# Optimization experiments

Hardware: AMD Instinct MI355X
Metric: run time of the kernel (lower is better)

## Reference

```python
import math
import jax, jax.numpy as jnp
import numpy as np

B, T = 2, 2048
D_MODEL, D_HEAD = 2048, 128
N_Q, N_KV = 16, 4
QPG = N_Q // N_KV  # queries per kv group
ROPE_BASE = 10000.0
YARN_SCALE = 4.0
ORIG_MAX_LEN = 4096
BETA_FAST, BETA_SLOW = 32.0, 1.0
RMS_EPS = 1.1920929e-07  # torch.finfo(float32).eps (nn.RMSNorm default)


def _yarn_inv_freq():
    inv = 1.0 / ROPE_BASE ** (np.arange(0, D_HEAD, 2, dtype=np.float32) / D_HEAD)
    wavelengths = 2.0 * math.pi / inv
    low_wavelen = ORIG_MAX_LEN / BETA_SLOW
    high_wavelen = ORIG_MAX_LEN / BETA_FAST
    gamma = np.clip((low_wavelen - wavelengths) / (low_wavelen - high_wavelen), 0.0, 1.0)
    return (gamma * inv + (1.0 - gamma) * inv / YARN_SCALE).astype(np.float32)

INV_FREQ = jnp.asarray(_yarn_inv_freq())  # (D_HEAD//2,) constant buffer
MSCALE = 0.1 * math.log(YARN_SCALE) + 1.0
ATTN_SCALE = 1.0 / (MSCALE * math.sqrt(D_HEAD))


def _rms_norm(x, w):
    # normalize over last dim (d_head), learnable per-dim weight
    return x * jax.lax.rsqrt(jnp.mean(x * x, axis=-1, keepdims=True) + RMS_EPS) * w


def _apply_rope(x):
    # x: (..., T, d_head)
    t = jnp.arange(x.shape[-2], dtype=jnp.float32)
    freqs = jnp.outer(t, INV_FREQ)                 # (T, d/2)
    emb = jnp.concatenate([freqs, freqs], axis=-1)  # (T, d)
    cos, sin = jnp.cos(emb), jnp.sin(emb)
    half = x.shape[-1] // 2
    x_rot = jnp.concatenate([-x[..., half:], x[..., :half]], axis=-1)
    return x * cos + x_rot * sin


def setup_inputs() -> dict:
    key = jax.random.key(0)
    ks = jax.random.split(key, 5)
    x = jax.random.normal(ks[0], (B, T, D_MODEL), dtype=jnp.float32)
    w_scale = 0.02
    Wq = jax.random.normal(ks[1], (D_MODEL, N_Q * D_HEAD), dtype=jnp.float32) * w_scale
    Wkv = jax.random.normal(ks[2], (D_MODEL, 2 * N_KV * D_HEAD), dtype=jnp.float32) * w_scale
    Wo = jax.random.normal(ks[3], (N_Q * D_HEAD, D_MODEL), dtype=jnp.float32) * w_scale
    q_norm_w = jnp.ones((D_HEAD,), dtype=jnp.float32)
    k_norm_w = jnp.ones((D_HEAD,), dtype=jnp.float32)
    return {"x": x, "Wq": Wq, "Wkv": Wkv, "Wo": Wo,
            "q_norm_w": q_norm_w, "k_norm_w": k_norm_w}


def reference(x, Wq, Wkv, Wo, q_norm_w, k_norm_w):
    b, t, _ = x.shape
    # projections
    q = (x @ Wq).reshape(b, t, QPG, N_KV, D_HEAD).transpose(0, 2, 3, 1, 4)  # (b,qpg,g,t,d)
    kv = x @ Wkv
    k, v = jnp.split(kv, 2, axis=-1)
    k = k.reshape(b, t, N_KV, D_HEAD).transpose(0, 2, 1, 3)  # (b,g,t,d)
    v = v.reshape(b, t, N_KV, D_HEAD).transpose(0, 2, 1, 3)  # (b,g,t,d)
    # RMSNorm + YaRN RoPE on q,k (math done in float32 as in source)
    q = _apply_rope(_rms_norm(q, q_norm_w))
    k = _apply_rope(_rms_norm(k, k_norm_w))
    # GQA replication: head index h = qpg*N_KV + g (matches source rearrange/reshape)
    q = q.reshape(b, N_Q, t, D_HEAD)
    k = jnp.broadcast_to(k[:, None], (b, QPG, N_KV, t, D_HEAD)).reshape(b, N_Q, t, D_HEAD)
    v = jnp.broadcast_to(v[:, None], (b, QPG, N_KV, t, D_HEAD)).reshape(b, N_Q, t, D_HEAD)
    # causal SDPA with custom scale
    scores = jnp.einsum('bhtd,bhsd->bhts', q, k) * ATTN_SCALE
    causal = jnp.tril(jnp.ones((t, t), dtype=bool))
    scores = jnp.where(causal, scores, jnp.finfo(scores.dtype).min)
    probs = jax.nn.softmax(scores, axis=-1)
    attn = jnp.einsum('bhts,bhsd->bhtd', probs, v)
    out = attn.transpose(0, 2, 1, 3).reshape(b, t, N_Q * D_HEAD)
    return out @ Wo
```

## Files before the change

### kernel.cpp

```cpp
#include <hip/hip_runtime.h>
#include <cmath>

typedef float f32x4 __attribute__((ext_vector_type(4)));
typedef float f32x16 __attribute__((ext_vector_type(16)));
typedef __bf16 bf16x8 __attribute__((ext_vector_type(8)));

#define DEV static __device__ __forceinline__

DEV unsigned short f2bf(float f) {
  unsigned int u = __builtin_bit_cast(unsigned int, f);
  u += 0x7FFFu + ((u >> 16) & 1u);
  return (unsigned short)(u >> 16);
}
DEV float bf2f(unsigned short h) {
  unsigned int u = ((unsigned int)h) << 16;
  return __builtin_bit_cast(float, u);
}
DEV unsigned int cvtpk(float lo, float hi) {
  unsigned int r;
  asm("v_cvt_pk_bf16_f32 %0, %1, %2" : "=v"(r) : "v"(lo), "v"(hi));
  return r;
}
DEV f32x4 mfma16(bf16x8 a, bf16x8 b, f32x4 c) {
  return __builtin_amdgcn_mfma_f32_16x16x32_bf16(a, b, c, 0, 0, 0);
}
DEV f32x16 mfma32(bf16x8 a, bf16x8 b, f32x16 c) {
  return __builtin_amdgcn_mfma_f32_32x32x16_bf16(a, b, c, 0, 0, 0);
}
DEV void dma16(const void* g, void* l) {
  __builtin_amdgcn_global_load_lds(
      (const __attribute__((address_space(1))) void*)(uintptr_t)g,
      (__attribute__((address_space(3))) void*)(unsigned int)(uintptr_t)l,
      16, 0, 0);
}

constexpr int T_SEQ = 2048;

__global__ __launch_bounds__(256) void build_rope(float2* __restrict__ rope) {
  int gid = blockIdx.x * 256 + threadIdx.x;
  if (gid >= T_SEQ * 64) return;
  int t = gid >> 6, i = gid & 63;
  double inv = pow(10000.0, -((double)(2 * i)) / 128.0);
  double wl = 6.283185307179586 / inv;
  double gm = (4096.0 - wl) / (4096.0 - 128.0);
  gm = gm < 0.0 ? 0.0 : (gm > 1.0 ? 1.0 : gm);
  float f = (float)(gm * inv + (1.0 - gm) * inv * 0.25);
  float th = (float)t * f;
  float s, c;
  sincosf(th, &s, &c);
  rope[gid] = make_float2(c, s);
}

__global__ __launch_bounds__(256) void cvt_f32_bf16(const float4* __restrict__ in,
                                                    ushort* __restrict__ out, int n4) {
  int i = blockIdx.x * 256 + threadIdx.x;
  if (i >= n4) return;
  float4 v = in[i];
  unsigned int lo = (unsigned int)f2bf(v.x) | ((unsigned int)f2bf(v.y) << 16);
  unsigned int hi = (unsigned int)f2bf(v.z) | ((unsigned int)f2bf(v.w) << 16);
  int row = i >> 9;
  int e = (i * 4) & 2047;
  size_t o = ((size_t)row << 11) + (size_t)(e ^ ((row & 7) << 3));
  *(uint2*)(out + o) = make_uint2(lo, hi);
}

__global__ __launch_bounds__(256) void tconv(const float* __restrict__ in,
                                             ushort* __restrict__ out, int R, int C) {
  __shared__ ushort tile[64][65];
  int c0 = blockIdx.x * 64, r0 = blockIdx.y * 64;
  int j = threadIdx.x & 63, i0 = threadIdx.x >> 6;
#pragma unroll
  for (int ii = 0; ii < 16; ++ii) {
    int i = i0 + ii * 4;
    tile[i][j] = f2bf(in[(size_t)(r0 + i) * C + c0 + j]);
  }
  __syncthreads();
#pragma unroll
  for (int ii = 0; ii < 16; ++ii) {
    int jr = i0 + ii * 4;
    out[(size_t)(c0 + jr) * R + ((r0 + j) ^ ((jr & 7) << 3))] = tile[j][jr];
  }
}

template <int OUT_BF16>
__global__ __launch_bounds__(256) void gemm_bt(const ushort* __restrict__ A,
                                               const ushort* __restrict__ Bt,
                                               void* __restrict__ Cv,
                                               int M, int N, int K) {
  __shared__ ushort lA[128 * 64];
  __shared__ ushort lB[128 * 64];
  const int tid = threadIdx.x;
  const int lane = tid & 63;
  const int w = tid >> 6;
  const int m0 = blockIdx.y * 128;
  const int n0 = blockIdx.x * 128;
  const int wm = (w >> 1) << 6;
  const int wn = (w & 1) << 6;

  f32x4 acc[4][4] = {};

  const size_t K2 = (size_t)K * 2;
  const char* Ab = (const char*)A + (size_t)m0 * K2;
  const char* Bb = (const char*)Bt + (size_t)n0 * K2;
  const int drow = w * 32 + (lane >> 3);
  const int dcb = (lane & 7) * 16;

  for (int k0 = 0; k0 < K; k0 += 64) {
#pragma unroll
    for (int ii = 0; ii < 4; ++ii) {
      const int off = w * 4096 + ii * 1024;
      const size_t gofs = (size_t)(drow + ii * 8) * K2 + (size_t)k0 * 2 + dcb;
      dma16(Ab + gofs, (char*)lA + off);
      dma16(Bb + gofs, (char*)lB + off);
    }
    __syncthreads();
#pragma unroll
    for (int kc = 0; kc < 2; ++kc) {
      bf16x8 a[4], bb[4];
#pragma unroll
      for (int mt = 0; mt < 4; ++mt) {
        int row = wm + mt * 16 + (lane & 15);
        int byo = kc * 64 + ((lane >> 4) << 4);
        a[mt] = *(const bf16x8*)((const char*)lA + row * 128 + (byo ^ ((row & 7) << 4)));
      }
#pragma unroll
      for (int nt = 0; nt < 4; ++nt) {
        int row = wn + nt * 16 + (lane & 15);
        int byo = kc * 64 + ((lane >> 4) << 4);
        bb[nt] = *(const bf16x8*)((const char*)lB + row * 128 + (byo ^ ((row & 7) << 4)));
      }
#pragma unroll
      for (int mt = 0; mt < 4; ++mt)
#pragma unroll
        for (int nt = 0; nt < 4; ++nt)
          acc[mt][nt] = mfma16(a[mt], bb[nt], acc[mt][nt]);
    }
    __syncthreads();
  }

  const int rr = (lane >> 4) << 2;
  const int cc = lane & 15;
  if (OUT_BF16) {
    ushort* C = (ushort*)Cv;
#pragma unroll
    for (int mt = 0; mt < 4; ++mt)
#pragma unroll
      for (int nt = 0; nt < 4; ++nt)
#pragma unroll
        for (int j = 0; j < 4; ++j) {
          int r = m0 + wm + mt * 16 + rr + j;
          int c = n0 + wn + nt * 16 + cc;
          C[(size_t)r * N + c] = f2bf(acc[mt][nt][j]);
        }
  } else {
    float* C = (float*)Cv;
#pragma unroll
    for (int mt = 0; mt < 4; ++mt)
#pragma unroll
      for (int nt = 0; nt < 4; ++nt)
#pragma unroll
        for (int j = 0; j < 4; ++j) {
          int r = m0 + wm + mt * 16 + rr + j;
          int c = n0 + wn + nt * 16 + cc;
          C[(size_t)r * N + c] = acc[mt][nt][j];
        }
  }
}

__global__ __launch_bounds__(256) void norm_rope(const ushort* __restrict__ qkv,
                                                 const float* __restrict__ qw,
                                                 const float* __restrict__ kw,
                                                 const float2* __restrict__ rope,
                                                 ushort* __restrict__ qout,
                                                 ushort* __restrict__ kout,
                                                 float q_scale) {
  const int w = threadIdx.x >> 6, lane = threadIdx.x & 63;
  const int vi = blockIdx.x * 4 + w;
  const ushort* src;
  const float* wt;
  ushort* dst;
  float extra;
  int t, bb;
  if (vi < 65536) {
    int row = vi >> 4, H = vi & 15;
    bb = row >> 11;
    t = row & 2047;
    src = qkv + (size_t)row * 3072 + H * 128 + lane * 2;
    wt = qw;
    extra = q_scale;
    dst = qout + ((size_t)(bb * 16 + H) * T_SEQ + t) * 128 + lane * 2;
  } else {
    int vi2 = vi - 65536;
    int row = vi2 >> 2, gg = vi2 & 3;
    bb = row >> 11;
    t = row & 2047;
    src = qkv + (size_t)row * 3072 + 2048 + gg * 128 + lane * 2;
    wt = kw;
    extra = 1.f;
    dst = kout + ((size_t)(bb * 4 + gg) * T_SEQ + t) * 128 +
          ((lane * 2) ^ ((t & 7) << 3));
  }
  float x0 = bf2f(src[0]), x1 = bf2f(src[1]);
  float ss = x0 * x0 + x1 * x1;
#pragma unroll
  for (int d = 1; d < 64; d <<= 1) ss += __shfl_xor(ss, d, 64);
  float sc = rsqrtf(ss * (1.f / 128.f) + 1.1920929e-7f);
  float w0 = wt[lane * 2], w1 = wt[lane * 2 + 1];
  float xn0 = x0 * sc * w0, xn1 = x1 * sc * w1;
  float p0 = __shfl_xor(xn0, 32, 64), p1 = __shfl_xor(xn1, 32, 64);
  float r0 = lane < 32 ? -p0 : p0;
  float r1 = lane < 32 ? -p1 : p1;
  int i0 = (lane * 2) & 63;
  float2 cs0 = rope[t * 64 + i0];
  float2 cs1 = rope[t * 64 + i0 + 1];
  float o0 = (xn0 * cs0.x + r0 * cs0.y) * extra;
  float o1 = (xn1 * cs1.x + r1 * cs1.y) * extra;
  unsigned int pk = (unsigned int)f2bf(o0) | ((unsigned int)f2bf(o1) << 16);
  *(unsigned int*)dst = pk;
}

__global__ __launch_bounds__(256) void tv_kernel(const ushort* __restrict__ qkv,
                                                 ushort* __restrict__ vt) {
  __shared__ ushort tile[64][65];
  int t0 = blockIdx.x * 64;
  int y = blockIdx.y;
  int dh = y & 1, bg = y >> 1;
  int bb = bg >> 2, g = bg & 3;
  int j = threadIdx.x & 63, i0 = threadIdx.x >> 6;
#pragma unroll
  for (int ii = 0; ii < 16; ++ii) {
    int i = i0 + ii * 4;
    tile[i][j] = qkv[(size_t)(bb * T_SEQ + t0 + i) * 3072 + 2560 + g * 128 + dh * 64 + j];
  }
  __syncthreads();
#pragma unroll
  for (int ii = 0; ii < 16; ++ii) {
    int jr = i0 + ii * 4;
    vt[((size_t)bg * 128 + dh * 64 + jr) * T_SEQ + ((t0 + j) ^ ((jr & 7) << 3))] = tile[j][jr];
  }
}

#define MKPA(P, B)                                                      \
  ({                                                                    \
    unsigned X1 = cvtpk(P[B + 0], P[B + 1]);                            \
    unsigned X2 = cvtpk(P[B + 2], P[B + 3]);                            \
    unsigned Y1 = cvtpk(P[B + 4], P[B + 5]);                            \
    unsigned Y2 = cvtpk(P[B + 6], P[B + 7]);                            \
    asm("v_permlane32_swap_b32 %0, %1" : "+v"(X1), "+v"(Y1));           \
    asm("v_permlane32_swap_b32 %0, %1" : "+v"(X2), "+v"(Y2));           \
    uint4 u4 = {X1, X2, Y1, Y2};                                        \
    __builtin_bit_cast(bf16x8, u4);                                     \
  })

__global__ __launch_bounds__(256, 2) void attn_fwd(const ushort* __restrict__ qh,
                                                   const ushort* __restrict__ kh,
                                                   const ushort* __restrict__ vt,
                                                   ushort* __restrict__ o) {
  const int f = blockIdx.x;
  const int half = f >> 8, c = f & 255;
  const int kk = c >> 5, bh = c & 31;
  const int qt = half ? kk : (15 - kk);
  const int b = bh >> 4, H = bh & 15;
  const int g = H & 3;
  const int tid = threadIdx.x, lane = tid & 63, w = tid >> 6;
  const int hi = lane >> 5;
  const int ql = lane & 31;
  const int wrow0 = qt * 128 + w * 32;

  __shared__ ushort lK[2][64 * 128];
  __shared__ ushort lV[2][128 * 64];

  bf16x8 qf[8];
  {
    const ushort* qb = qh + ((size_t)(b * 16 + H) * T_SEQ + wrow0 + ql) * 128 + 8 * hi;
#pragma unroll
    for (int cc = 0; cc < 8; ++cc) qf[cc] = *(const bf16x8*)(qb + 16 * cc);
  }

  f32x16 oacc[4] = {};
  float mrow = -INFINITY, lrow = 0.f;

  const char* kpl = (const char*)(kh + (size_t)(b * 4 + g) * T_SEQ * 128);
  const char* vpl = (const char*)(vt + (size_t)(b * 4 + g) * 128 * T_SEQ);

  auto stage = [&](int j, int bi) {
#pragma unroll
    for (int ii = 0; ii < 4; ++ii) {
      const int off = w * 4096 + ii * 1024;
      dma16(kpl + (size_t)j * 16384 + off + lane * 16, (char*)lK[bi] + off);
      const int vrow = w * 32 + ii * 8 + (lane >> 3);
      dma16(vpl + (size_t)vrow * (T_SEQ * 2) + j * 128 + (lane & 7) * 16,
            (char*)lV[bi] + off);
    }
  };

  stage(0, 0);

  const int swK = (ql & 7) << 4;
  const int jmax = 2 * qt + 1;

  for (int j = 0; j <= jmax; ++j) {
    const int cur = j & 1;
    if (j < jmax) {
      stage(j + 1, cur ^ 1);
      asm volatile("s_waitcnt vmcnt(8)" ::: "memory");
    } else {
      asm volatile("s_waitcnt vmcnt(0)" ::: "memory");
    }
    __builtin_amdgcn_s_barrier();
    __builtin_amdgcn_sched_barrier(0);

    const char* lKc = (const char*)lK[cur];
    const char* lVc = (const char*)lV[cur];

    f32x16 s0 = {}, s1 = {};
    __builtin_amdgcn_s_setprio(1);
#pragma unroll
    for (int cc = 0; cc < 8; ++cc) {
      bf16x8 kf = *(const bf16x8*)(lKc + ql * 256 + ((32 * cc + 16 * hi) ^ swK));
      s0 = mfma32(kf, qf[cc], s0);
    }
#pragma unroll
    for (int cc = 0; cc < 8; ++cc) {
      bf16x8 kf = *(const bf16x8*)(lKc + (32 + ql) * 256 + ((32 * cc + 16 * hi) ^ swK));
      s1 = mfma32(kf, qf[cc], s1);
    }
    __builtin_amdgcn_s_setprio(0);

    if (j * 64 + 63 > wrow0) {
      const int q = wrow0 + ql;
      const int kvb = j * 64 + 4 * hi;
#pragma unroll
      for (int r = 0; r < 16; ++r) {
        const int kv0 = kvb + (r & 3) + 8 * (r >> 2);
        if (kv0 > q) s0[r] = -3.0e38f;
        if (kv0 + 32 > q) s1[r] = -3.0e38f;
      }
    }

    float tm[8];
#pragma unroll
    for (int r = 0; r < 8; ++r)
      tm[r] = fmaxf(fmaxf(s0[r], s0[r + 8]), fmaxf(s1[r], s1[r + 8]));
    float pm = fmaxf(fmaxf(fmaxf(tm[0], tm[1]), fmaxf(tm[2], tm[3])),
                     fmaxf(fmaxf(tm[4], tm[5]), fmaxf(tm[6], tm[7])));
    pm = fmaxf(pm, __shfl_xor(pm, 32, 64));

    float mn = mrow;
    if (!__all(pm <= mrow + 11.5417f)) {
      mn = fmaxf(mrow, pm);
      float rsc = exp2f(mrow - mn);
      mrow = mn;
      lrow *= rsc;
#pragma unroll
      for (int r = 0; r < 16; ++r) {
        float rv = __shfl(rsc, (r & 3) + 8 * (r >> 2) + 4 * hi, 64);
#pragma unroll
        for (int n = 0; n < 4; ++n) oacc[n][r] *= rv;
      }
    }

    f32x16 p0, p1;
#pragma unroll
    for (int r = 0; r < 16; ++r) {
      p0[r] = exp2f(s0[r] - mn);
      p1[r] = exp2f(s1[r] - mn);
    }
    float ta[8];
#pragma unroll
    for (int r = 0; r < 8; ++r) ta[r] = (p0[r] + p0[r + 8]) + (p1[r] + p1[r + 8]);
    float ps = ((ta[0] + ta[1]) + (ta[2] + ta[3])) + ((ta[4] + ta[5]) + (ta[6] + ta[7]));
    ps += __shfl_xor(ps, 32, 64);
    lrow += ps;

    bf16x8 pa0 = MKPA(p0, 0), pa1 = MKPA(p0, 8);
    bf16x8 pa2 = MKPA(p1, 0), pa3 = MKPA(p1, 8);

    __builtin_amdgcn_s_setprio(1);
#pragma unroll
    for (int n = 0; n < 4; ++n) {
      const int row = 32 * n + ql;
      const int swV = (row & 7) << 4;
      const char* vb = lVc + row * 128;
      bf16x8 vf0 = *(const bf16x8*)(vb + ((16 * hi) ^ swV));
      bf16x8 vf1 = *(const bf16x8*)(vb + ((32 + 16 * hi) ^ swV));
      bf16x8 vf2 = *(const bf16x8*)(vb + ((64 + 16 * hi) ^ swV));
      bf16x8 vf3 = *(const bf16x8*)(vb + ((96 + 16 * hi) ^ swV));
      oacc[n] = mfma32(pa0, vf0, oacc[n]);
      oacc[n] = mfma32(pa1, vf1, oacc[n]);
      oacc[n] = mfma32(pa2, vf2, oacc[n]);
      oacc[n] = mfma32(pa3, vf3, oacc[n]);
    }
    __builtin_amdgcn_s_setprio(0);

    __builtin_amdgcn_sched_barrier(0);
    __builtin_amdgcn_s_barrier();
  }

  float linv = 1.f / lrow;
#pragma unroll
  for (int r = 0; r < 16; ++r) {
    const int qrr = (r & 3) + 8 * (r >> 2) + 4 * hi;
    float iv = __shfl(linv, qrr, 64);
    const int row = wrow0 + qrr;
    const size_t base = (size_t)(b * T_SEQ + row) * 2048;
    const int sw = (row & 7) << 3;
#pragma unroll
    for (int n = 0; n < 4; ++n) {
      int col = H * 128 + n * 32 + ql;
      o[base + (col ^ sw)] = f2bf(oacc[n][r] * iv);
    }
  }
}

extern "C" void kernel_launch(void* const* d_in, const int* in_sizes, int n_in,
                              void* d_out, int out_size, void* d_ws, size_t ws_size,
                              hipStream_t stream) {
  (void)in_sizes; (void)n_in; (void)out_size; (void)ws_size;
  const float* x = (const float*)d_in[0];
  const float* Wq = (const float*)d_in[1];
  const float* Wkv = (const float*)d_in[2];
  const float* Wo = (const float*)d_in[3];
  const float* qnw = (const float*)d_in[4];
  const float* knw = (const float*)d_in[5];
  float* out = (float*)d_out;
  char* ws = (char*)d_ws;

  ushort* xb = (ushort*)(ws);
  ushort* wqkv = (ushort*)(ws + 16777216);
  ushort* wot = (ushort*)(ws + 29360128);
  ushort* qkvraw = (ushort*)(ws + 37748736);
  ushort* kh = (ushort*)(ws + 62914560);
  ushort* vtp = (ushort*)(ws + 67108864);
  float2* rope = (float2*)(ws + 71303168);
  ushort* qh = xb;
  ushort* attnb = qkvraw;

  float attn_scale = 1.0f / ((0.1f * logf(4.0f) + 1.0f) * sqrtf(128.0f));
  float q_scale = attn_scale * 1.44269504f;

  build_rope<<<512, 256, 0, stream>>>(rope);
  cvt_f32_bf16<<<8192, 256, 0, stream>>>((const float4*)x, xb, 2097152);
  tconv<<<dim3(32, 32), 256, 0, stream>>>(Wq, wqkv, 2048, 2048);
  tconv<<<dim3(16, 32), 256, 0, stream>>>(Wkv, wqkv + (size_t)2048 * 2048, 2048, 1024);
  tconv<<<dim3(32, 32), 256, 0, stream>>>(Wo, wot, 2048, 2048);
  gemm_bt<1><<<dim3(24, 32), 256, 0, stream>>>(xb, wqkv, qkvraw, 4096, 3072, 2048);
  norm_rope<<<20480, 256, 0, stream>>>(qkvraw, qnw, knw, rope, qh, kh, q_scale);
  tv_kernel<<<dim3(32, 16), 256, 0, stream>>>(qkvraw, vtp);
  attn_fwd<<<512, 256, 0, stream>>>(qh, kh, vtp, attnb);
  gemm_bt<0><<<dim3(16, 32), 256, 0, stream>>>(attnb, wot, out, 4096, 2048, 2048);
}
```

Measured before the change: 228.6 us.

## Replace LDS-staged attention with single-wave blocks reading K/V from global

Attention is restructured from 256-thread blocks that double-buffer 64-key K/V tiles into shared memory via async DMA into 2048 single-wave blocks, each handling 32 query rows and reading 32-key K/V tiles straight from global memory. The shared-memory XOR swizzles on K and transposed V are removed from the producer kernels to match. This drops block barriers and LDS traffic and makes causal tiling finer, at the cost of no K/V reuse across the four waves of a block, more global/L2 traffic and exposed load latency without prefetch.

```diff
diff --git a/kernel.cpp b/kernel.cpp
--- a/kernel.cpp
+++ b/kernel.cpp
@@ -197,8 +197,7 @@
     src = qkv + (size_t)row * 3072 + 2048 + gg * 128 + lane * 2;
     wt = kw;
     extra = 1.f;
-    dst = kout + ((size_t)(bb * 4 + gg) * T_SEQ + t) * 128 +
-          ((lane * 2) ^ ((t & 7) << 3));
+    dst = kout + ((size_t)(bb * 4 + gg) * T_SEQ + t) * 128 + lane * 2;
   }
   float x0 = bf2f(src[0]), x1 = bf2f(src[1]);
   float ss = x0 * x0 + x1 * x1;
@@ -236,7 +235,7 @@
 #pragma unroll
   for (int ii = 0; ii < 16; ++ii) {
     int jr = i0 + ii * 4;
-    vt[((size_t)bg * 128 + dh * 64 + jr) * T_SEQ + ((t0 + j) ^ ((jr & 7) << 3))] = tile[j][jr];
+    vt[((size_t)bg * 128 + dh * 64 + jr) * T_SEQ + t0 + j] = tile[j][jr];
   }
 }
 
@@ -252,27 +251,23 @@
     __builtin_bit_cast(bf16x8, u4);                                     \
   })
 
-__global__ __launch_bounds__(256, 2) void attn_fwd(const ushort* __restrict__ qh,
-                                                   const ushort* __restrict__ kh,
-                                                   const ushort* __restrict__ vt,
-                                                   ushort* __restrict__ o) {
+__global__ __launch_bounds__(64) void attn_fwd(const ushort* __restrict__ qh,
+                                               const ushort* __restrict__ kh,
+                                               const ushort* __restrict__ vt,
+                                               ushort* __restrict__ o) {
   const int f = blockIdx.x;
-  const int half = f >> 8, c = f & 255;
-  const int kk = c >> 5, bh = c & 31;
-  const int qt = half ? kk : (15 - kk);
+  const int qs = 63 - (f >> 5);
+  const int bh = f & 31;
   const int b = bh >> 4, H = bh & 15;
   const int g = H & 3;
-  const int tid = threadIdx.x, lane = tid & 63, w = tid >> 6;
+  const int lane = threadIdx.x;
   const int hi = lane >> 5;
   const int ql = lane & 31;
-  const int wrow0 = qt * 128 + w * 32;
-
-  __shared__ ushort lK[2][64 * 128];
-  __shared__ ushort lV[2][128 * 64];
+  const int row0 = qs * 32;
 
   bf16x8 qf[8];
   {
-    const ushort* qb = qh + ((size_t)(b * 16 + H) * T_SEQ + wrow0 + ql) * 128 + 8 * hi;
+    const ushort* qb = qh + ((size_t)(b * 16 + H) * T_SEQ + row0 + ql) * 128 + 8 * hi;
 #pragma unroll
     for (int cc = 0; cc < 8; ++cc) qf[cc] = *(const bf16x8*)(qb + 16 * cc);
   }
@@ -280,68 +275,34 @@
   f32x16 oacc[4] = {};
   float mrow = -INFINITY, lrow = 0.f;
 
-  const char* kpl = (const char*)(kh + (size_t)(b * 4 + g) * T_SEQ * 128);
-  const char* vpl = (const char*)(vt + (size_t)(b * 4 + g) * 128 * T_SEQ);
-
-  auto stage = [&](int j, int bi) {
-#pragma unroll
-    for (int ii = 0; ii < 4; ++ii) {
-      const int off = w * 4096 + ii * 1024;
-      dma16(kpl + (size_t)j * 16384 + off + lane * 16, (char*)lK[bi] + off);
-      const int vrow = w * 32 + ii * 8 + (lane >> 3);
-      dma16(vpl + (size_t)vrow * (T_SEQ * 2) + j * 128 + (lane & 7) * 16,
-            (char*)lV[bi] + off);
-    }
-  };
-
-  stage(0, 0);
-
-  const int swK = (ql & 7) << 4;
-  const int jmax = 2 * qt + 1;
-
-  for (int j = 0; j <= jmax; ++j) {
-    const int cur = j & 1;
-    if (j < jmax) {
-      stage(j + 1, cur ^ 1);
-      asm volatile("s_waitcnt vmcnt(8)" ::: "memory");
-    } else {
-      asm volatile("s_waitcnt vmcnt(0)" ::: "memory");
-    }
-    __builtin_amdgcn_s_barrier();
-    __builtin_amdgcn_sched_barrier(0);
-
-    const char* lKc = (const char*)lK[cur];
-    const char* lVc = (const char*)lV[cur];
-
-    f32x16 s0 = {}, s1 = {};
+  const char* kb = (const char*)(kh + (size_t)(b * 4 + g) * T_SEQ * 128);
+  const char* vb = (const char*)(vt + (size_t)(b * 4 + g) * 128 * T_SEQ);
+
+  const int q = row0 + ql;
+
+  for (int kt = 0; kt <= qs; ++kt) {
+    const char* kp = kb + (size_t)kt * 8192 + ql * 256 + hi * 16;
+    f32x16 s = {};
     __builtin_amdgcn_s_setprio(1);
 #pragma unroll
     for (int cc = 0; cc < 8; ++cc) {
-      bf16x8 kf = *(const bf16x8*)(lKc + ql * 256 + ((32 * cc + 16 * hi) ^ swK));
-      s0 = mfma32(kf, qf[cc], s0);
-    }
-#pragma unroll
-    for (int cc = 0; cc < 8; ++cc) {
-      bf16x8 kf = *(const bf16x8*)(lKc + (32 + ql) * 256 + ((32 * cc + 16 * hi) ^ swK));
-      s1 = mfma32(kf, qf[cc], s1);
+      bf16x8 kf = *(const bf16x8*)(kp + cc * 32);
+      s = mfma32(kf, qf[cc], s);
     }
     __builtin_amdgcn_s_setprio(0);
 
-    if (j * 64 + 63 > wrow0) {
-      const int q = wrow0 + ql;
-      const int kvb = j * 64 + 4 * hi;
+    if (kt == qs) {
+      const int cb = 4 * hi;
 #pragma unroll
       for (int r = 0; r < 16; ++r) {
-        const int kv0 = kvb + (r & 3) + 8 * (r >> 2);
-        if (kv0 > q) s0[r] = -3.0e38f;
-        if (kv0 + 32 > q) s1[r] = -3.0e38f;
+        const int cc2 = cb + (r & 3) + 8 * (r >> 2);
+        if (cc2 > ql) s[r] = -3.0e38f;
       }
     }
 
     float tm[8];
 #pragma unroll
-    for (int r = 0; r < 8; ++r)
-      tm[r] = fmaxf(fmaxf(s0[r], s0[r + 8]), fmaxf(s1[r], s1[r + 8]));
+    for (int r = 0; r < 8; ++r) tm[r] = fmaxf(s[r], s[r + 8]);
     float pm = fmaxf(fmaxf(fmaxf(tm[0], tm[1]), fmaxf(tm[2], tm[3])),
                      fmaxf(fmaxf(tm[4], tm[5]), fmaxf(tm[6], tm[7])));
     pm = fmaxf(pm, __shfl_xor(pm, 32, 64));
@@ -360,41 +321,28 @@
       }
     }
 
-    f32x16 p0, p1;
-#pragma unroll
-    for (int r = 0; r < 16; ++r) {
-      p0[r] = exp2f(s0[r] - mn);
-      p1[r] = exp2f(s1[r] - mn);
-    }
+    f32x16 p;
+#pragma unroll
+    for (int r = 0; r < 16; ++r) p[r] = exp2f(s[r] - mn);
     float ta[8];
 #pragma unroll
-    for (int r = 0; r < 8; ++r) ta[r] = (p0[r] + p0[r + 8]) + (p1[r] + p1[r + 8]);
+    for (int r = 0; r < 8; ++r) ta[r] = p[r] + p[r + 8];
     float ps = ((ta[0] + ta[1]) + (ta[2] + ta[3])) + ((ta[4] + ta[5]) + (ta[6] + ta[7]));
     ps += __shfl_xor(ps, 32, 64);
     lrow += ps;
 
-    bf16x8 pa0 = MKPA(p0, 0), pa1 = MKPA(p0, 8);
-    bf16x8 pa2 = MKPA(p1, 0), pa3 = MKPA(p1, 8);
+    bf16x8 pa_lo = MKPA(p, 0), pa_hi = MKPA(p, 8);
 
     __builtin_amdgcn_s_setprio(1);
 #pragma unroll
     for (int n = 0; n < 4; ++n) {
-      const int row = 32 * n + ql;
-      const int swV = (row & 7) << 4;
-      const char* vb = lVc + row * 128;
-      bf16x8 vf0 = *(const bf16x8*)(vb + ((16 * hi) ^ swV));
-      bf16x8 vf1 = *(const bf16x8*)(vb + ((32 + 16 * hi) ^ swV));
-      bf16x8 vf2 = *(const bf16x8*)(vb + ((64 + 16 * hi) ^ swV));
-      bf16x8 vf3 = *(const bf16x8*)(vb + ((96 + 16 * hi) ^ swV));
-      oacc[n] = mfma32(pa0, vf0, oacc[n]);
-      oacc[n] = mfma32(pa1, vf1, oacc[n]);
-      oacc[n] = mfma32(pa2, vf2, oacc[n]);
-      oacc[n] = mfma32(pa3, vf3, oacc[n]);
+      const char* vp = vb + (size_t)(32 * n + ql) * 4096 + kt * 64 + hi * 16;
+      bf16x8 vf_lo = *(const bf16x8*)(vp);
+      bf16x8 vf_hi = *(const bf16x8*)(vp + 32);
+      oacc[n] = mfma32(pa_lo, vf_lo, oacc[n]);
+      oacc[n] = mfma32(pa_hi, vf_hi, oacc[n]);
     }
     __builtin_amdgcn_s_setprio(0);
-
-    __builtin_amdgcn_sched_barrier(0);
-    __builtin_amdgcn_s_barrier();
   }
 
   float linv = 1.f / lrow;
@@ -402,7 +350,7 @@
   for (int r = 0; r < 16; ++r) {
     const int qrr = (r & 3) + 8 * (r >> 2) + 4 * hi;
     float iv = __shfl(linv, qrr, 64);
-    const int row = wrow0 + qrr;
+    const int row = row0 + qrr;
     const size_t base = (size_t)(b * T_SEQ + row) * 2048;
     const int sw = (row & 7) << 3;
 #pragma unroll
@@ -447,6 +395,6 @@
   gemm_bt<1><<<dim3(24, 32), 256, 0, stream>>>(xb, wqkv, qkvraw, 4096, 3072, 2048);
   norm_rope<<<20480, 256, 0, stream>>>(qkvraw, qnw, knw, rope, qh, kh, q_scale);
   tv_kernel<<<dim3(32, 16), 256, 0, stream>>>(qkvraw, vtp);
-  attn_fwd<<<512, 256, 0, stream>>>(qh, kh, vtp, attnb);
+  attn_fwd<<<2048, 64, 0, stream>>>(qh, kh, vtp, attnb);
   gemm_bt<0><<<dim3(16, 32), 256, 0, stream>>>(attnb, wot, out, 4096, 2048, 2048);
 }
```

After: 304.5 us. +33.2%, slower.

## Pair complementary causal query tiles per attention block with 512-thread blocks

Applied to the files above, without the earlier changes.

The attention kernel now launches 256 blocks of 512 threads. Each block processes two 256-row query tiles, tileA and its mirror 7-tileA, one after the other, so every block does the same total causal work. The K/V staging pipeline runs continuously across both tiles, with the online-softmax state reset and Q reloaded between them. Waves whose rows lie wholly above the current KV tile skip compute but still join barriers. Intra-block load imbalance rises because of those idle waves, and the grid halves to 256 blocks, which may underfill the CUs.

```diff
diff --git a/kernel.cpp b/kernel.cpp
--- a/kernel.cpp
+++ b/kernel.cpp
@@ -252,165 +252,197 @@
     __builtin_bit_cast(bf16x8, u4);                                     \
   })
 
-__global__ __launch_bounds__(256, 2) void attn_fwd(const ushort* __restrict__ qh,
+__global__ __launch_bounds__(512, 2) void attn_fwd(const ushort* __restrict__ qh,
                                                    const ushort* __restrict__ kh,
                                                    const ushort* __restrict__ vt,
                                                    ushort* __restrict__ o) {
   const int f = blockIdx.x;
-  const int half = f >> 8, c = f & 255;
-  const int kk = c >> 5, bh = c & 31;
-  const int qt = half ? kk : (15 - kk);
+  const int bh = f & 31;
+  const int tA = f >> 3 & 7;
   const int b = bh >> 4, H = bh & 15;
   const int g = H & 3;
   const int tid = threadIdx.x, lane = tid & 63, w = tid >> 6;
   const int hi = lane >> 5;
   const int ql = lane & 31;
-  const int wrow0 = qt * 128 + w * 32;
+
+  const int tileA = f >> 5;
+  const int tileB = 7 - tileA;
+  (void)tA;
 
   __shared__ ushort lK[2][64 * 128];
   __shared__ ushort lV[2][128 * 64];
 
-  bf16x8 qf[8];
-  {
-    const ushort* qb = qh + ((size_t)(b * 16 + H) * T_SEQ + wrow0 + ql) * 128 + 8 * hi;
-#pragma unroll
-    for (int cc = 0; cc < 8; ++cc) qf[cc] = *(const bf16x8*)(qb + 16 * cc);
-  }
+  const char* kpl = (const char*)(kh + (size_t)(b * 4 + g) * T_SEQ * 128);
+  const char* vpl = (const char*)(vt + (size_t)(b * 4 + g) * 128 * T_SEQ);
+
+  auto stage = [&](int j, int bi) {
+#pragma unroll
+    for (int ii = 0; ii < 2; ++ii) {
+      const int off = w * 2048 + ii * 1024;
+      dma16(kpl + (size_t)j * 16384 + off + lane * 16, (char*)lK[bi] + off);
+      const int vrow = w * 16 + ii * 8 + (lane >> 3);
+      dma16(vpl + (size_t)vrow * (T_SEQ * 2) + j * 128 + (lane & 7) * 16,
+            (char*)lV[bi] + off);
+    }
+  };
 
   f32x16 oacc[4] = {};
   float mrow = -INFINITY, lrow = 0.f;
-
-  const char* kpl = (const char*)(kh + (size_t)(b * 4 + g) * T_SEQ * 128);
-  const char* vpl = (const char*)(vt + (size_t)(b * 4 + g) * 128 * T_SEQ);
-
-  auto stage = [&](int j, int bi) {
-#pragma unroll
-    for (int ii = 0; ii < 4; ++ii) {
-      const int off = w * 4096 + ii * 1024;
-      dma16(kpl + (size_t)j * 16384 + off + lane * 16, (char*)lK[bi] + off);
-      const int vrow = w * 32 + ii * 8 + (lane >> 3);
-      dma16(vpl + (size_t)vrow * (T_SEQ * 2) + j * 128 + (lane & 7) * 16,
-            (char*)lV[bi] + off);
-    }
+  bf16x8 qf[8];
+
+  const int swK = (ql & 7) << 4;
+
+  auto load_q = [&](int tbase_) {
+    const ushort* qb =
+        qh + ((size_t)(b * 16 + H) * T_SEQ + tbase_ + w * 32 + ql) * 128 + 8 * hi;
+#pragma unroll
+    for (int cc = 0; cc < 8; ++cc) qf[cc] = *(const bf16x8*)(qb + 16 * cc);
   };
 
+  auto epilogue = [&](int tbase_) {
+    float linv = 1.f / lrow;
+#pragma unroll
+    for (int r = 0; r < 16; ++r) {
+      const int qrr = (r & 3) + 8 * (r >> 2) + 4 * hi;
+      float iv = __shfl(linv, qrr, 64);
+      const int row = tbase_ + w * 32 + qrr;
+      const size_t base = (size_t)(b * T_SEQ + row) * 2048;
+      const int sw = (row & 7) << 3;
+#pragma unroll
+      for (int n = 0; n < 4; ++n) {
+        int col = H * 128 + n * 32 + ql;
+        o[base + (col ^ sw)] = f2bf(oacc[n][r] * iv);
+      }
+    }
+  };
+
+  const int jmA = 4 * tileA + 3, jmB = 4 * tileB + 3;
+  const int NIT = jmA + jmB + 2;
+
+  int tbase = tileA * 256;
+  int jloc0 = 0, jmaxcur = jmA;
+  load_q(tbase);
+
   stage(0, 0);
 
-  const int swK = (ql & 7) << 4;
-  const int jmax = 2 * qt + 1;
-
-  for (int j = 0; j <= jmax; ++j) {
-    const int cur = j & 1;
-    if (j < jmax) {
-      stage(j + 1, cur ^ 1);
-      asm volatile("s_waitcnt vmcnt(8)" ::: "memory");
+  for (int i = 0; i < NIT; ++i) {
+    const int cur = i & 1;
+    const int jloc = i - jloc0;
+    if (i + 1 < NIT) {
+      int nj = i + 1 - jloc0;
+      int sj = (nj > jmaxcur) ? 0 : nj;
+      stage(sj, cur ^ 1);
+      asm volatile("s_waitcnt vmcnt(4)" ::: "memory");
     } else {
       asm volatile("s_waitcnt vmcnt(0)" ::: "memory");
     }
     __builtin_amdgcn_s_barrier();
     __builtin_amdgcn_sched_barrier(0);
 
-    const char* lKc = (const char*)lK[cur];
-    const char* lVc = (const char*)lV[cur];
-
-    f32x16 s0 = {}, s1 = {};
-    __builtin_amdgcn_s_setprio(1);
-#pragma unroll
-    for (int cc = 0; cc < 8; ++cc) {
-      bf16x8 kf = *(const bf16x8*)(lKc + ql * 256 + ((32 * cc + 16 * hi) ^ swK));
-      s0 = mfma32(kf, qf[cc], s0);
-    }
-#pragma unroll
-    for (int cc = 0; cc < 8; ++cc) {
-      bf16x8 kf = *(const bf16x8*)(lKc + (32 + ql) * 256 + ((32 * cc + 16 * hi) ^ swK));
-      s1 = mfma32(kf, qf[cc], s1);
-    }
-    __builtin_amdgcn_s_setprio(0);
-
-    if (j * 64 + 63 > wrow0) {
-      const int q = wrow0 + ql;
-      const int kvb = j * 64 + 4 * hi;
+    const int wrow0 = tbase + w * 32;
+    const bool act = (jloc * 64 <= wrow0 + 31);
+    if (act) {
+      const char* lKc = (const char*)lK[cur];
+      const char* lVc = (const char*)lV[cur];
+
+      f32x16 s0 = {}, s1 = {};
+      __builtin_amdgcn_s_setprio(1);
+#pragma unroll
+      for (int cc = 0; cc < 8; ++cc) {
+        bf16x8 kf = *(const bf16x8*)(lKc + ql * 256 + ((32 * cc + 16 * hi) ^ swK));
+        s0 = mfma32(kf, qf[cc], s0);
+      }
+#pragma unroll
+      for (int cc = 0; cc < 8; ++cc) {
+        bf16x8 kf = *(const bf16x8*)(lKc + (32 + ql) * 256 + ((32 * cc + 16 * hi) ^ swK));
+        s1 = mfma32(kf, qf[cc], s1);
+      }
+      __builtin_amdgcn_s_setprio(0);
+
+      if (jloc * 64 + 63 > wrow0) {
+        const int q = wrow0 + ql;
+        const int kvb = jloc * 64 + 4 * hi;
+#pragma unroll
+        for (int r = 0; r < 16; ++r) {
+          const int kv0 = kvb + (r & 3) + 8 * (r >> 2);
+          if (kv0 > q) s0[r] = -3.0e38f;
+          if (kv0 + 32 > q) s1[r] = -3.0e38f;
+        }
+      }
+
+      float tm[8];
+#pragma unroll
+      for (int r = 0; r < 8; ++r)
+        tm[r] = fmaxf(fmaxf(s0[r], s0[r + 8]), fmaxf(s1[r], s1[r + 8]));
+      float pm = fmaxf(fmaxf(fmaxf(tm[0], tm[1]), fmaxf(tm[2], tm[3])),
+                       fmaxf(fmaxf(tm[4], tm[5]), fmaxf(tm[6], tm[7])));
+      pm = fmaxf(pm, __shfl_xor(pm, 32, 64));
+
+      float mn = mrow;
+      if (!__all(pm <= mrow + 11.5417f)) {
+        mn = fmaxf(mrow, pm);
+        float rsc = exp2f(mrow - mn);
+        mrow = mn;
+        lrow *= rsc;
+#pragma unroll
+        for (int r = 0; r < 16; ++r) {
+          float rv = __shfl(rsc, (r & 3) + 8 * (r >> 2) + 4 * hi, 64);
+#pragma unroll
+          for (int n = 0; n < 4; ++n) oacc[n][r] *= rv;
+        }
+      }
+
+      f32x16 p0, p1;
 #pragma unroll
       for (int r = 0; r < 16; ++r) {
-        const int kv0 = kvb + (r & 3) + 8 * (r >> 2);
-        if (kv0 > q) s0[r] = -3.0e38f;
-        if (kv0 + 32 > q) s1[r] = -3.0e38f;
-      }
-    }
-
-    float tm[8];
-#pragma unroll
-    for (int r = 0; r < 8; ++r)
-      tm[r] = fmaxf(fmaxf(s0[r], s0[r + 8]), fmaxf(s1[r], s1[r + 8]));
-    float pm = fmaxf(fmaxf(fmaxf(tm[0], tm[1]), fmaxf(tm[2], tm[3])),
-                     fmaxf(fmaxf(tm[4], tm[5]), fmaxf(tm[6], tm[7])));
-    pm = fmaxf(pm, __shfl_xor(pm, 32, 64));
-
-    float mn = mrow;
-    if (!__all(pm <= mrow + 11.5417f)) {
-      mn = fmaxf(mrow, pm);
-      float rsc = exp2f(mrow - mn);
-      mrow = mn;
-      lrow *= rsc;
-#pragma unroll
-      for (int r = 0; r < 16; ++r) {
-        float rv = __shfl(rsc, (r & 3) + 8 * (r >> 2) + 4 * hi, 64);
-#pragma unroll
-        for (int n = 0; n < 4; ++n) oacc[n][r] *= rv;
-      }
-    }
-
-    f32x16 p0, p1;
-#pragma unroll
-    for (int r = 0; r < 16; ++r) {
-      p0[r] = exp2f(s0[r] - mn);
-      p1[r] = exp2f(s1[r] - mn);
-    }
-    float ta[8];
-#pragma unroll
-    for (int r = 0; r < 8; ++r) ta[r] = (p0[r] + p0[r + 8]) + (p1[r] + p1[r + 8]);
-    float ps = ((ta[0] + ta[1]) + (ta[2] + ta[3])) + ((ta[4] + ta[5]) + (ta[6] + ta[7]));
-    ps += __shfl_xor(ps, 32, 64);
-    lrow += ps;
-
-    bf16x8 pa0 = MKPA(p0, 0), pa1 = MKPA(p0, 8);
-    bf16x8 pa2 = MKPA(p1, 0), pa3 = MKPA(p1, 8);
-
-    __builtin_amdgcn_s_setprio(1);
-#pragma unroll
-    for (int n = 0; n < 4; ++n) {
-      const int row = 32 * n + ql;
-      const int swV = (row & 7) << 4;
-      const char* vb = lVc + row * 128;
-      bf16x8 vf0 = *(const bf16x8*)(vb + ((16 * hi) ^ swV));
-      bf16x8 vf1 = *(const bf16x8*)(vb + ((32 + 16 * hi) ^ swV));
-      bf16x8 vf2 = *(const bf16x8*)(vb + ((64 + 16 * hi) ^ swV));
-      bf16x8 vf3 = *(const bf16x8*)(vb + ((96 + 16 * hi) ^ swV));
-      oacc[n] = mfma32(pa0, vf0, oacc[n]);
-      oacc[n] = mfma32(pa1, vf1, oacc[n]);
-      oacc[n] = mfma32(pa2, vf2, oacc[n]);
-      oacc[n] = mfma32(pa3, vf3, oacc[n]);
-    }
-    __builtin_amdgcn_s_setprio(0);
+        p0[r] = exp2f(s0[r] - mn);
+        p1[r] = exp2f(s1[r] - mn);
+      }
+      float ta[8];
+#pragma unroll
+      for (int r = 0; r < 8; ++r) ta[r] = (p0[r] + p0[r + 8]) + (p1[r] + p1[r + 8]);
+      float ps = ((ta[0] + ta[1]) + (ta[2] + ta[3])) + ((ta[4] + ta[5]) + (ta[6] + ta[7]));
+      ps += __shfl_xor(ps, 32, 64);
+      lrow += ps;
+
+      bf16x8 pa0 = MKPA(p0, 0), pa1 = MKPA(p0, 8);
+      bf16x8 pa2 = MKPA(p1, 0), pa3 = MKPA(p1, 8);
+
+      __builtin_amdgcn_s_setprio(1);
+#pragma unroll
+      for (int n = 0; n < 4; ++n) {
+        const int row = 32 * n + ql;
+        const int swV = (row & 7) << 4;
+        const char* vb = lVc + row * 128;
+        bf16x8 vf0 = *(const bf16x8*)(vb + ((16 * hi) ^ swV));
+        bf16x8 vf1 = *(const bf16x8*)(vb + ((32 + 16 * hi) ^ swV));
+        bf16x8 vf2 = *(const bf16x8*)(vb + ((64 + 16 * hi) ^ swV));
+        bf16x8 vf3 = *(const bf16x8*)(vb + ((96 + 16 * hi) ^ swV));
+        oacc[n] = mfma32(pa0, vf0, oacc[n]);
+        oacc[n] = mfma32(pa1, vf1, oacc[n]);
+        oacc[n] = mfma32(pa2, vf2, oacc[n]);
+        oacc[n] = mfma32(pa3, vf3, oacc[n]);
+      }
+      __builtin_amdgcn_s_setprio(0);
+    }
 
     __builtin_amdgcn_sched_barrier(0);
     __builtin_amdgcn_s_barrier();
-  }
-
-  float linv = 1.f / lrow;
-#pragma unroll
-  for (int r = 0; r < 16; ++r) {
-    const int qrr = (r & 3) + 8 * (r >> 2) + 4 * hi;
-    float iv = __shfl(linv, qrr, 64);
-    const int row = wrow0 + qrr;
-    const size_t base = (size_t)(b * T_SEQ + row) * 2048;
-    const int sw = (row & 7) << 3;
-#pragma unroll
-    for (int n = 0; n < 4; ++n) {
-      int col = H * 128 + n * 32 + ql;
-      o[base + (col ^ sw)] = f2bf(oacc[n][r] * iv);
-    }
-  }
+
+    if (i == jmA) {
+      epilogue(tbase);
+#pragma unroll
+      for (int n = 0; n < 4; ++n) oacc[n] = f32x16{};
+      mrow = -INFINITY;
+      lrow = 0.f;
+      tbase = tileB * 256;
+      jloc0 = jmA + 1;
+      jmaxcur = jmB;
+      load_q(tbase);
+    }
+  }
+
+  epilogue(tbase);
 }
 
 extern "C" void kernel_launch(void* const* d_in, const int* in_sizes, int n_in,
@@ -447,6 +479,6 @@
   gemm_bt<1><<<dim3(24, 32), 256, 0, stream>>>(xb, wqkv, qkvraw, 4096, 3072, 2048);
   norm_rope<<<20480, 256, 0, stream>>>(qkvraw, qnw, knw, rope, qh, kh, q_scale);
   tv_kernel<<<dim3(32, 16), 256, 0, stream>>>(qkvraw, vtp);
-  attn_fwd<<<512, 256, 0, stream>>>(qh, kh, vtp, attnb);
+  attn_fwd<<<256, 512, 0, stream>>>(qh, kh, vtp, attnb);
   gemm_bt<0><<<dim3(16, 32), 256, 0, stream>>>(attnb, wot, out, 4096, 2048, 2048);
 }
```

Measured after the change: 305.4 us. 33.6% more time.
